# Performance work log

Measured on AMD Instinct MI355X. Metric: run time of the kernel, lower is better.

The kernel has to match this reference:

```python
import jax, jax.numpy as jnp
import numpy as np

N_NODES = 50000
F_IN = 96
HIDDEN = 128
OUT = 64
N_EDGES = 800000


def setup_inputs() -> dict:
    key = jax.random.key(0)
    ks = jax.random.split(key, 8)
    x = jax.random.normal(ks[0], (N_NODES, F_IN), dtype=jnp.float32)
    edge_index = jax.random.randint(ks[1], (2, N_EDGES), 0, N_NODES, dtype=jnp.int64)
    s = 1.0 / np.sqrt(F_IN)
    W1_rel = jax.random.uniform(ks[2], (HIDDEN, F_IN), minval=-s, maxval=s, dtype=jnp.float32)
    b1 = jax.random.uniform(ks[3], (HIDDEN,), minval=-s, maxval=s, dtype=jnp.float32)
    W1_root = jax.random.uniform(ks[4], (HIDDEN, F_IN), minval=-s, maxval=s, dtype=jnp.float32)
    s2 = 1.0 / np.sqrt(HIDDEN)
    W2_rel = jax.random.uniform(ks[5], (OUT, HIDDEN), minval=-s2, maxval=s2, dtype=jnp.float32)
    b2 = jax.random.uniform(ks[6], (OUT,), minval=-s2, maxval=s2, dtype=jnp.float32)
    W2_root = jax.random.uniform(ks[7], (OUT, HIDDEN), minval=-s2, maxval=s2, dtype=jnp.float32)
    return {"x": x, "edge_index": edge_index, "W1_rel": W1_rel, "b1": b1,
            "W1_root": W1_root, "W2_rel": W2_rel, "b2": b2, "W2_root": W2_root}


def _graph_conv(x, src, dst, mask, W_rel, b, W_root):
    # messages = x[src] (masked to remove self-loops), sum-aggregated at dst
    msgs = x[src] * mask  # [E, F]
    agg = jax.ops.segment_sum(msgs, dst, num_segments=x.shape[0])  # [N, F]
    return agg @ W_rel.T + b + x @ W_root.T


def reference(x, edge_index, W1_rel, b1, W1_root, W2_rel, b2, W2_root):
    src, dst = edge_index[0], edge_index[1]
    # remove_self_loops: zero out contributions of edges with src == dst
    mask = (src != dst).astype(x.dtype)[:, None]  # [E, 1]
    h = jax.nn.relu(_graph_conv(x, src, dst, mask, W1_rel, b1, W1_root))
    out = _graph_conv(h, src, dst, mask, W2_rel, b2, W2_root)
    return out
```

## Files before the change

### kernel.cpp

```cpp
#include <hip/hip_runtime.h>


#define N_NODES 50000
#define F_IN    96
#define HIDDEN  128
#define OUT_F   64
#define DCAP    64

typedef __attribute__((ext_vector_type(8))) short short8;
typedef __attribute__((ext_vector_type(4))) float floatx4;

__device__ inline unsigned short f2bf(float f) {
    union { float f; unsigned u; } v; v.f = f;
    unsigned r = v.u + 0x7FFF + ((v.u >> 16) & 1);
    return (unsigned short)(r >> 16);
}
__device__ inline float bf2f(unsigned short b) {
    union { unsigned u; float f; } v; v.u = ((unsigned)b) << 16;
    return v.f;
}

__global__ __launch_bounds__(256) void setup_place_kernel(
    const float* __restrict__ x,
    const float* __restrict__ W1_rel, const float* __restrict__ W1_root,
    const float* __restrict__ W2_rel, const float* __restrict__ W2_root,
    const int* __restrict__ ei,
    unsigned short* __restrict__ xb, unsigned short* __restrict__ W1b,
    unsigned short* __restrict__ W2rb, unsigned short* __restrict__ W2sb,
    int* __restrict__ deg, int* __restrict__ csr,
    int SB, int total8, int E, int slice_size)
{
    const int tid = threadIdx.x;
    if ((int)blockIdx.x < SB) {
        int i = blockIdx.x * 256 + tid;
        if (i < total8) {
            const float4* p = (const float4*)(x + (size_t)i * 8);
            float4 v0 = p[0], v1 = p[1];
            short8 o;
            o[0] = (short)f2bf(v0.x); o[1] = (short)f2bf(v0.y);
            o[2] = (short)f2bf(v0.z); o[3] = (short)f2bf(v0.w);
            o[4] = (short)f2bf(v1.x); o[5] = (short)f2bf(v1.y);
            o[6] = (short)f2bf(v1.z); o[7] = (short)f2bf(v1.w);
            *(short8*)(xb + (size_t)i * 8) = o;
        }
        if (i < 128 * 192) {
            int j = i / 192, k = i % 192;
            float v = (k < 96) ? W1_rel[j * 96 + k] : W1_root[j * 96 + k - 96];
            W1b[i] = f2bf(v);
        } else if (i < 128 * 192 + 64 * 128) {
            int i2 = i - 128 * 192;
            W2rb[i2] = f2bf(W2_rel[i2]);
        } else if (i < 128 * 192 + 2 * 64 * 128) {
            int i3 = i - 128 * 192 - 64 * 128;
            W2sb[i3] = f2bf(W2_root[i3]);
        }
        return;
    }
    int pb = blockIdx.x - SB;
    int sl = pb & 7;
    int i4 = (pb >> 3) * 256 + tid;
    int E4 = E >> 2;
    if (i4 < E4) {
        int4 d4 = ((const int4*)(ei + E))[i4];
        int e0 = i4 * 4;
        int dd[4] = {d4.x, d4.y, d4.z, d4.w};
        #pragma unroll
        for (int k = 0; k < 4; ++k) {
            int d = dd[k];
            if ((unsigned)d >= (unsigned)N_NODES) continue;
            if (d / slice_size != sl) continue;
            int s = ei[e0 + k];
            if (s == d) continue;
            int r = atomicAdd(&deg[d], 1);
            if (r < DCAP) csr[d * DCAP + r] = s;
        }
    } else if (i4 == E4) {
        for (int e = E4 * 4; e < E; ++e) {
            int d = ei[E + e];
            if ((unsigned)d >= (unsigned)N_NODES) continue;
            if (d / slice_size != sl) continue;
            int s = ei[e];
            if (s == d) continue;
            int r = atomicAdd(&deg[d], 1);
            if (r < DCAP) csr[d * DCAP + r] = s;
        }
    }
}

template<int F>
__device__ inline void gather_row8(const unsigned short* __restrict__ feat,
                                   const int* __restrict__ csr, int j, int end,
                                   float* acc)
{
    const unsigned short* fc = feat;
    for (; j + 3 < end; j += 4) {
        int s0 = csr[j], s1 = csr[j + 1], s2 = csr[j + 2], s3 = csr[j + 3];
        s0 = ((unsigned)s0 < (unsigned)N_NODES) ? s0 : 0;
        s1 = ((unsigned)s1 < (unsigned)N_NODES) ? s1 : 0;
        s2 = ((unsigned)s2 < (unsigned)N_NODES) ? s2 : 0;
        s3 = ((unsigned)s3 < (unsigned)N_NODES) ? s3 : 0;
        short8 v0 = *(const short8*)(fc + (size_t)s0 * F);
        short8 v1 = *(const short8*)(fc + (size_t)s1 * F);
        short8 v2 = *(const short8*)(fc + (size_t)s2 * F);
        short8 v3 = *(const short8*)(fc + (size_t)s3 * F);
        #pragma unroll
        for (int i = 0; i < 8; ++i)
            acc[i] += (bf2f((unsigned short)v0[i]) + bf2f((unsigned short)v1[i]))
                    + (bf2f((unsigned short)v2[i]) + bf2f((unsigned short)v3[i]));
    }
    for (; j < end; ++j) {
        int s0 = csr[j];
        s0 = ((unsigned)s0 < (unsigned)N_NODES) ? s0 : 0;
        short8 v0 = *(const short8*)(fc + (size_t)s0 * F);
        #pragma unroll
        for (int i = 0; i < 8; ++i) acc[i] += bf2f((unsigned short)v0[i]);
    }
}

__global__ __launch_bounds__(256) void mega1_kernel(
    const unsigned short* __restrict__ xb, const unsigned short* __restrict__ W1b,
    const unsigned short* __restrict__ W2rb, const float* __restrict__ b1,
    const int* __restrict__ deg, const int* __restrict__ csr,
    unsigned short* __restrict__ h, unsigned short* __restrict__ t, int N)
{
    __shared__ __align__(16) unsigned short aggs[32][104];
    __shared__ __align__(16) unsigned short hs[32][136];
    const int tid = threadIdx.x;
    const int node0 = blockIdx.x * 32;

    for (int task = tid; task < 384; task += 256) {
        int nl = task / 12, c = task % 12;
        int node = node0 + nl;
        float acc[8] = {};
        if (node < N) {
            int dg = deg[node];
            if (dg > DCAP) dg = DCAP;
            int j = node * DCAP;
            gather_row8<F_IN>(xb + c * 8, csr, j, j + dg, acc);
        }
        short8 o;
        #pragma unroll
        for (int i = 0; i < 8; ++i) o[i] = (short)f2bf(acc[i]);
        *(short8*)&aggs[nl][c * 8] = o;
    }
    __syncthreads();

    const int lane = tid & 63;
    const int wave = tid >> 6;
    const int m = lane & 15, quad = lane >> 4;
    const int nh = wave & 1;
    const int node_base = node0 + nh * 16;
    const int jt0 = (wave >> 1) * 4;
    int na = node_base + m;
    if (na >= N) na = N - 1;
    short8 a[6];
    #pragma unroll
    for (int c = 0; c < 3; ++c)
        a[c] = *(const short8*)&aggs[nh * 16 + m][c * 32 + quad * 8];
    #pragma unroll
    for (int c = 0; c < 3; ++c)
        a[3 + c] = *(const short8*)(xb + (size_t)na * 96 + c * 32 + quad * 8);
    #pragma unroll
    for (int jt = 0; jt < 4; ++jt) {
        floatx4 acc = {0.f, 0.f, 0.f, 0.f};
        const unsigned short* wb = W1b + (size_t)((jt0 + jt) * 16 + m) * 192 + quad * 8;
        #pragma unroll
        for (int c = 0; c < 6; ++c) {
            short8 b = *(const short8*)(wb + c * 32);
            acc = __builtin_amdgcn_mfma_f32_16x16x32_bf16(a[c], b, acc, 0, 0, 0);
        }
        int col = (jt0 + jt) * 16 + m;
        float bv = b1[col];
        #pragma unroll
        for (int r = 0; r < 4; ++r) {
            int node = node_base + quad * 4 + r;
            float v = fmaxf(acc[r] + bv, 0.f);
            unsigned short vb = f2bf(v);
            hs[nh * 16 + quad * 4 + r][col] = vb;
            if (node < N) h[(size_t)node * 128 + col] = vb;
        }
    }
    __syncthreads();

    const int jtt0 = (wave >> 1) * 2;
    short8 a2[4];
    #pragma unroll
    for (int c = 0; c < 4; ++c)
        a2[c] = *(const short8*)&hs[nh * 16 + m][c * 32 + quad * 8];
    #pragma unroll
    for (int jt = 0; jt < 2; ++jt) {
        floatx4 acc = {0.f, 0.f, 0.f, 0.f};
        const unsigned short* wb = W2rb + (size_t)((jtt0 + jt) * 16 + m) * 128 + quad * 8;
        #pragma unroll
        for (int c = 0; c < 4; ++c) {
            short8 b = *(const short8*)(wb + c * 32);
            acc = __builtin_amdgcn_mfma_f32_16x16x32_bf16(a2[c], b, acc, 0, 0, 0);
        }
        int col = (jtt0 + jt) * 16 + m;
        #pragma unroll
        for (int r = 0; r < 4; ++r) {
            int node = node_base + quad * 4 + r;
            if (node < N)
                t[(size_t)node * 64 + col] = f2bf(acc[r]);
        }
    }
}

__global__ __launch_bounds__(256) void gemm3_fused(
    const unsigned short* __restrict__ h, const unsigned short* __restrict__ tfeat,
    const unsigned short* __restrict__ W2sb, const float* __restrict__ b2,
    const int* __restrict__ deg, const int* __restrict__ csr,
    float* __restrict__ out, int N)
{
    __shared__ __align__(16) unsigned short agg2s[32][72];
    const int tid = threadIdx.x;
    const int node0 = blockIdx.x * 32;

    {
        int nl = tid / 8, c = tid % 8;
        int node = node0 + nl;
        float acc[8] = {};
        if (node < N) {
            int dg = deg[node];
            if (dg > DCAP) dg = DCAP;
            int j = node * DCAP;
            gather_row8<OUT_F>(tfeat + c * 8, csr, j, j + dg, acc);
        }
        short8 o;
        #pragma unroll
        for (int i = 0; i < 8; ++i) o[i] = (short)f2bf(acc[i]);
        *(short8*)&agg2s[nl][c * 8] = o;
    }
    __syncthreads();

    const int lane = tid & 63;
    const int wave = tid >> 6;
    const int m = lane & 15, quad = lane >> 4;
    const int node_base = node0 + (wave & 1) * 16;
    const int jt0 = (wave >> 1) * 2;
    int na = node_base + m;
    if (na >= N) na = N - 1;
    short8 a[4];
    #pragma unroll
    for (int c = 0; c < 4; ++c)
        a[c] = *(const short8*)(h + (size_t)na * 128 + c * 32 + quad * 8);
    #pragma unroll
    for (int jt = 0; jt < 2; ++jt) {
        floatx4 acc = {0.f, 0.f, 0.f, 0.f};
        const unsigned short* wb = W2sb + (size_t)((jt0 + jt) * 16 + m) * 128 + quad * 8;
        #pragma unroll
        for (int c = 0; c < 4; ++c) {
            short8 b = *(const short8*)(wb + c * 32);
            acc = __builtin_amdgcn_mfma_f32_16x16x32_bf16(a[c], b, acc, 0, 0, 0);
        }
        int col = (jt0 + jt) * 16 + m;
        float bv = b2[col];
        #pragma unroll
        for (int r = 0; r < 4; ++r) {
            int node = node_base + quad * 4 + r;
            if (node < N) {
                int nl = (wave & 1) * 16 + quad * 4 + r;
                float v = acc[r] + bv + bf2f(agg2s[nl][col]);
                out[(size_t)node * 64 + col] = v;
            }
        }
    }
}

extern "C" void kernel_launch(void* const* d_in, const int* in_sizes, int n_in,
                              void* d_out, int out_size, void* d_ws, size_t ws_size,
                              hipStream_t stream) {
    const float* x       = (const float*)d_in[0];
    const int*   ei      = (const int*)d_in[1];
    const float* W1_rel  = (const float*)d_in[2];
    const float* b1      = (const float*)d_in[3];
    const float* W1_root = (const float*)d_in[4];
    const float* W2_rel  = (const float*)d_in[5];
    const float* b2      = (const float*)d_in[6];
    const float* W2_root = (const float*)d_in[7];
    float* out = (float*)d_out;

    const int N = in_sizes[0] / F_IN;
    const int E = in_sizes[1] / 2;
    const int slice_size = ((N + 2047) / 2048) * 256;

    char* ws = (char*)d_ws;
    size_t p = 0;
    unsigned short* xb   = (unsigned short*)(ws + p); p += (size_t)N_NODES * F_IN * 2;
    unsigned short* h    = (unsigned short*)(ws + p); p += (size_t)N_NODES * HIDDEN * 2;
    unsigned short* t    = (unsigned short*)(ws + p); p += (size_t)N_NODES * OUT_F * 2;
    unsigned short* W1b  = (unsigned short*)(ws + p); p += (size_t)128 * 192 * 2;
    unsigned short* W2rb = (unsigned short*)(ws + p); p += (size_t)64 * 128 * 2;
    unsigned short* W2sb = (unsigned short*)(ws + p); p += (size_t)64 * 128 * 2;
    int* deg = (int*)(ws + p);  p += (size_t)N_NODES * 4;
    int* csr = (int*)(ws + p);  p += (size_t)N_NODES * DCAP * 4;

    hipMemsetAsync(deg, 0, (size_t)N * 4, stream);

    {
        int total8 = N * F_IN / 8;
        int SB = (total8 + 255) / 256;
        int E4 = E >> 2;
        int bps = (E4 + 1 + 255) / 256;
        int PB = bps * 8;
        setup_place_kernel<<<SB + PB, 256, 0, stream>>>(
            x, W1_rel, W1_root, W2_rel, W2_root, ei,
            xb, W1b, W2rb, W2sb, deg, csr, SB, total8, E, slice_size);
    }

    const int tiles32 = (N + 31) / 32;

    mega1_kernel<<<tiles32, 256, 0, stream>>>(xb, W1b, W2rb, b1, deg, csr, h, t, N);

    gemm3_fused<<<tiles32, 256, 0, stream>>>(h, t, W2sb, b2, deg, csr, out, N);
}
```

Baseline: 201.0 us.

## Split gathers into XCD-aware kernels over 32-column feature slabs

Feature matrices are stored a second time as 32-column slabs, and the neighbor gathers move into a separate kernel. That kernel maps each XCD (via blockIdx & 7) to one slab, so each XCD's L2 holds a smaller working set of 3.2 MB rather than the full table. Each node's neighbor list is now split across 4 lanes and combined with shuffles, and csr indices are read with nontemporal loads. The cost is two extra kernel launches, extra global round trips for the aggregate buffers and a duplicated copy of x.

```diff
diff --git a/kernel.cpp b/kernel.cpp
--- a/kernel.cpp
+++ b/kernel.cpp
@@ -25,7 +25,8 @@
     const float* __restrict__ W1_rel, const float* __restrict__ W1_root,
     const float* __restrict__ W2_rel, const float* __restrict__ W2_root,
     const int* __restrict__ ei,
-    unsigned short* __restrict__ xb, unsigned short* __restrict__ W1b,
+    unsigned short* __restrict__ xb, unsigned short* __restrict__ xc,
+    unsigned short* __restrict__ W1b,
     unsigned short* __restrict__ W2rb, unsigned short* __restrict__ W2sb,
     int* __restrict__ deg, int* __restrict__ csr,
     int SB, int total8, int E, int slice_size)
@@ -42,6 +43,9 @@
             o[4] = (short)f2bf(v1.x); o[5] = (short)f2bf(v1.y);
             o[6] = (short)f2bf(v1.z); o[7] = (short)f2bf(v1.w);
             *(short8*)(xb + (size_t)i * 8) = o;
+            int node = i / 12, c = i % 12;
+            int slab = c >> 2, c2 = c & 3;
+            *(short8*)(xc + ((size_t)slab * N_NODES + node) * 32 + c2 * 8) = o;
         }
         if (i < 128 * 192) {
             int j = i / 192, k = i % 192;
@@ -87,64 +91,75 @@
     }
 }
 
-template<int F>
-__device__ inline void gather_row8(const unsigned short* __restrict__ feat,
-                                   const int* __restrict__ csr, int j, int end,
-                                   float* acc)
+template<int OUTSTRIDE>
+__global__ __launch_bounds__(512) void gather_kernel(
+    const unsigned short* __restrict__ fc,
+    const int* __restrict__ deg, const int* __restrict__ csr,
+    unsigned short* __restrict__ aggout, int N, int three_slabs)
 {
-    const unsigned short* fc = feat;
-    for (; j + 3 < end; j += 4) {
-        int s0 = csr[j], s1 = csr[j + 1], s2 = csr[j + 2], s3 = csr[j + 3];
-        s0 = ((unsigned)s0 < (unsigned)N_NODES) ? s0 : 0;
-        s1 = ((unsigned)s1 < (unsigned)N_NODES) ? s1 : 0;
-        s2 = ((unsigned)s2 < (unsigned)N_NODES) ? s2 : 0;
-        s3 = ((unsigned)s3 < (unsigned)N_NODES) ? s3 : 0;
-        short8 v0 = *(const short8*)(fc + (size_t)s0 * F);
-        short8 v1 = *(const short8*)(fc + (size_t)s1 * F);
-        short8 v2 = *(const short8*)(fc + (size_t)s2 * F);
-        short8 v3 = *(const short8*)(fc + (size_t)s3 * F);
-        #pragma unroll
-        for (int i = 0; i < 8; ++i)
-            acc[i] += (bf2f((unsigned short)v0[i]) + bf2f((unsigned short)v1[i]))
-                    + (bf2f((unsigned short)v2[i]) + bf2f((unsigned short)v3[i]));
-    }
-    for (; j < end; ++j) {
-        int s0 = csr[j];
-        s0 = ((unsigned)s0 < (unsigned)N_NODES) ? s0 : 0;
-        short8 v0 = *(const short8*)(fc + (size_t)s0 * F);
-        #pragma unroll
-        for (int i = 0; i < 8; ++i) acc[i] += bf2f((unsigned short)v0[i]);
-    }
-}
-
-__global__ __launch_bounds__(256) void mega1_kernel(
-    const unsigned short* __restrict__ xb, const unsigned short* __restrict__ W1b,
-    const unsigned short* __restrict__ W2rb, const float* __restrict__ b1,
-    const int* __restrict__ deg, const int* __restrict__ csr,
-    unsigned short* __restrict__ h, unsigned short* __restrict__ t, int N)
+    const int tid = threadIdx.x;
+    const int bid = blockIdx.x;
+    const int xcd = bid & 7;
+    const int k = bid >> 3;
+    int slab, rank, g;
+    if (three_slabs) { slab = xcd % 3; rank = xcd / 3; g = (slab == 2) ? 2 : 3; }
+    else             { slab = xcd & 1; rank = xcd >> 1; g = 4; }
+    const int ntiles = (N + 31) >> 5;
+    const int tile = k * g + rank;
+    if (tile >= ntiles) return;
+
+    const int c2 = tid & 3;
+    const int q  = (tid >> 2) & 3;
+    const int nl = tid >> 4;
+    const int node = tile * 32 + nl;
+    const unsigned short* sb = fc + (size_t)slab * N_NODES * 32 + c2 * 8;
+
+    float acc[8] = {};
+    if (node < N) {
+        int dg = deg[node]; if (dg > DCAP) dg = DCAP;
+        int j = node * DCAP + q;
+        const int end = node * DCAP + dg;
+        for (; j + 4 < end; j += 8) {
+            int s0 = __builtin_nontemporal_load(csr + j);
+            int s1 = __builtin_nontemporal_load(csr + j + 4);
+            s0 = ((unsigned)s0 < (unsigned)N_NODES) ? s0 : 0;
+            s1 = ((unsigned)s1 < (unsigned)N_NODES) ? s1 : 0;
+            short8 v0 = *(const short8*)(sb + (size_t)s0 * 32);
+            short8 v1 = *(const short8*)(sb + (size_t)s1 * 32);
+            #pragma unroll
+            for (int i = 0; i < 8; ++i)
+                acc[i] += bf2f((unsigned short)v0[i]) + bf2f((unsigned short)v1[i]);
+        }
+        if (j < end) {
+            int s0 = __builtin_nontemporal_load(csr + j);
+            s0 = ((unsigned)s0 < (unsigned)N_NODES) ? s0 : 0;
+            short8 v0 = *(const short8*)(sb + (size_t)s0 * 32);
+            #pragma unroll
+            for (int i = 0; i < 8; ++i) acc[i] += bf2f((unsigned short)v0[i]);
+        }
+    }
+    #pragma unroll
+    for (int i = 0; i < 8; ++i) {
+        acc[i] += __shfl_xor(acc[i], 4);
+        acc[i] += __shfl_xor(acc[i], 8);
+    }
+    if (q == 0 && node < N) {
+        short8 o;
+        #pragma unroll
+        for (int i = 0; i < 8; ++i) o[i] = (short)f2bf(acc[i]);
+        *(short8*)(aggout + (size_t)node * OUTSTRIDE + slab * 32 + c2 * 8) = o;
+    }
+}
+
+__global__ __launch_bounds__(256) void gemm12_kernel(
+    const unsigned short* __restrict__ xb, const unsigned short* __restrict__ aggb,
+    const unsigned short* __restrict__ W1b, const unsigned short* __restrict__ W2rb,
+    const float* __restrict__ b1,
+    unsigned short* __restrict__ h, unsigned short* __restrict__ tc, int N)
 {
-    __shared__ __align__(16) unsigned short aggs[32][104];
     __shared__ __align__(16) unsigned short hs[32][136];
     const int tid = threadIdx.x;
     const int node0 = blockIdx.x * 32;
-
-    for (int task = tid; task < 384; task += 256) {
-        int nl = task / 12, c = task % 12;
-        int node = node0 + nl;
-        float acc[8] = {};
-        if (node < N) {
-            int dg = deg[node];
-            if (dg > DCAP) dg = DCAP;
-            int j = node * DCAP;
-            gather_row8<F_IN>(xb + c * 8, csr, j, j + dg, acc);
-        }
-        short8 o;
-        #pragma unroll
-        for (int i = 0; i < 8; ++i) o[i] = (short)f2bf(acc[i]);
-        *(short8*)&aggs[nl][c * 8] = o;
-    }
-    __syncthreads();
-
     const int lane = tid & 63;
     const int wave = tid >> 6;
     const int m = lane & 15, quad = lane >> 4;
@@ -156,7 +171,7 @@
     short8 a[6];
     #pragma unroll
     for (int c = 0; c < 3; ++c)
-        a[c] = *(const short8*)&aggs[nh * 16 + m][c * 32 + quad * 8];
+        a[c] = *(const short8*)(aggb + (size_t)na * 96 + c * 32 + quad * 8);
     #pragma unroll
     for (int c = 0; c < 3; ++c)
         a[3 + c] = *(const short8*)(xb + (size_t)na * 96 + c * 32 + quad * 8);
@@ -197,42 +212,23 @@
             acc = __builtin_amdgcn_mfma_f32_16x16x32_bf16(a2[c], b, acc, 0, 0, 0);
         }
         int col = (jtt0 + jt) * 16 + m;
+        int slab = col >> 5, cw = col & 31;
         #pragma unroll
         for (int r = 0; r < 4; ++r) {
             int node = node_base + quad * 4 + r;
             if (node < N)
-                t[(size_t)node * 64 + col] = f2bf(acc[r]);
-        }
-    }
-}
-
-__global__ __launch_bounds__(256) void gemm3_fused(
-    const unsigned short* __restrict__ h, const unsigned short* __restrict__ tfeat,
+                tc[((size_t)slab * N_NODES + node) * 32 + cw] = f2bf(acc[r]);
+        }
+    }
+}
+
+__global__ __launch_bounds__(256) void gemm3_kernel(
+    const unsigned short* __restrict__ h, const unsigned short* __restrict__ agg2b,
     const unsigned short* __restrict__ W2sb, const float* __restrict__ b2,
-    const int* __restrict__ deg, const int* __restrict__ csr,
     float* __restrict__ out, int N)
 {
-    __shared__ __align__(16) unsigned short agg2s[32][72];
     const int tid = threadIdx.x;
     const int node0 = blockIdx.x * 32;
-
-    {
-        int nl = tid / 8, c = tid % 8;
-        int node = node0 + nl;
-        float acc[8] = {};
-        if (node < N) {
-            int dg = deg[node];
-            if (dg > DCAP) dg = DCAP;
-            int j = node * DCAP;
-            gather_row8<OUT_F>(tfeat + c * 8, csr, j, j + dg, acc);
-        }
-        short8 o;
-        #pragma unroll
-        for (int i = 0; i < 8; ++i) o[i] = (short)f2bf(acc[i]);
-        *(short8*)&agg2s[nl][c * 8] = o;
-    }
-    __syncthreads();
-
     const int lane = tid & 63;
     const int wave = tid >> 6;
     const int m = lane & 15, quad = lane >> 4;
@@ -244,6 +240,17 @@
     #pragma unroll
     for (int c = 0; c < 4; ++c)
         a[c] = *(const short8*)(h + (size_t)na * 128 + c * 32 + quad * 8);
+    float agv[2][4];
+    #pragma unroll
+    for (int jt = 0; jt < 2; ++jt) {
+        int col = (jt0 + jt) * 16 + m;
+        #pragma unroll
+        for (int r = 0; r < 4; ++r) {
+            int node = node_base + quad * 4 + r;
+            int nc = (node < N) ? node : (N - 1);
+            agv[jt][r] = bf2f(agg2b[(size_t)nc * 64 + col]);
+        }
+    }
     #pragma unroll
     for (int jt = 0; jt < 2; ++jt) {
         floatx4 acc = {0.f, 0.f, 0.f, 0.f};
@@ -258,11 +265,8 @@
         #pragma unroll
         for (int r = 0; r < 4; ++r) {
             int node = node_base + quad * 4 + r;
-            if (node < N) {
-                int nl = (wave & 1) * 16 + quad * 4 + r;
-                float v = acc[r] + bv + bf2f(agg2s[nl][col]);
-                out[(size_t)node * 64 + col] = v;
-            }
+            if (node < N)
+                out[(size_t)node * 64 + col] = acc[r] + bv + agv[jt][r];
         }
     }
 }
@@ -286,12 +290,15 @@
 
     char* ws = (char*)d_ws;
     size_t p = 0;
-    unsigned short* xb   = (unsigned short*)(ws + p); p += (size_t)N_NODES * F_IN * 2;
-    unsigned short* h    = (unsigned short*)(ws + p); p += (size_t)N_NODES * HIDDEN * 2;
-    unsigned short* t    = (unsigned short*)(ws + p); p += (size_t)N_NODES * OUT_F * 2;
-    unsigned short* W1b  = (unsigned short*)(ws + p); p += (size_t)128 * 192 * 2;
-    unsigned short* W2rb = (unsigned short*)(ws + p); p += (size_t)64 * 128 * 2;
-    unsigned short* W2sb = (unsigned short*)(ws + p); p += (size_t)64 * 128 * 2;
+    unsigned short* xb    = (unsigned short*)(ws + p); p += (size_t)N_NODES * F_IN * 2;
+    unsigned short* xc    = (unsigned short*)(ws + p); p += (size_t)3 * N_NODES * 32 * 2;
+    unsigned short* aggb  = (unsigned short*)(ws + p); p += (size_t)N_NODES * F_IN * 2;
+    unsigned short* h     = (unsigned short*)(ws + p); p += (size_t)N_NODES * HIDDEN * 2;
+    unsigned short* tc    = (unsigned short*)(ws + p); p += (size_t)2 * N_NODES * 32 * 2;
+    unsigned short* agg2b = (unsigned short*)(ws + p); p += (size_t)N_NODES * OUT_F * 2;
+    unsigned short* W1b   = (unsigned short*)(ws + p); p += (size_t)128 * 192 * 2;
+    unsigned short* W2rb  = (unsigned short*)(ws + p); p += (size_t)64 * 128 * 2;
+    unsigned short* W2sb  = (unsigned short*)(ws + p); p += (size_t)64 * 128 * 2;
     int* deg = (int*)(ws + p);  p += (size_t)N_NODES * 4;
     int* csr = (int*)(ws + p);  p += (size_t)N_NODES * DCAP * 4;
 
@@ -305,12 +312,22 @@
         int PB = bps * 8;
         setup_place_kernel<<<SB + PB, 256, 0, stream>>>(
             x, W1_rel, W1_root, W2_rel, W2_root, ei,
-            xb, W1b, W2rb, W2sb, deg, csr, SB, total8, E, slice_size);
-    }
-
-    const int tiles32 = (N + 31) / 32;
-
-    mega1_kernel<<<tiles32, 256, 0, stream>>>(xb, W1b, W2rb, b1, deg, csr, h, t, N);
-
-    gemm3_fused<<<tiles32, 256, 0, stream>>>(h, t, W2sb, b2, deg, csr, out, N);
-}
+            xb, xc, W1b, W2rb, W2sb, deg, csr, SB, total8, E, slice_size);
+    }
+
+    const int ntiles = (N + 31) / 32;
+
+    {
+        int g1k = (ntiles + 1) / 2;
+        gather_kernel<96><<<8 * g1k, 512, 0, stream>>>(xc, deg, csr, aggb, N, 1);
+    }
+
+    gemm12_kernel<<<ntiles, 256, 0, stream>>>(xb, aggb, W1b, W2rb, b1, h, tc, N);
+
+    {
+        int g2k = (ntiles + 3) / 4;
+        gather_kernel<64><<<8 * g2k, 512, 0, stream>>>(tc, deg, csr, agg2b, N, 0);
+    }
+
+    gemm3_kernel<<<ntiles, 256, 0, stream>>>(h, agg2b, W2sb, b2, out, N);
+}
```

Measured after the change: 234.3 us. 1.17x slower.

## Pack edge pairs into 16-bit words and store CSR indices as uint16

Applied to the files above, without the earlier changes.

Adds a pre-pass kernel that packs each (src,dst) pair into one 32-bit word and zeroes the degree array, which replaces the memset. The 8 placement slices then each read one packed array instead of the 64-bit index arrays, and the CSR neighbour lists are stored as 16-bit indices. Both gather kernels read half as many index bytes. This relies on N fitting in 16 bits (50000 < 65536), writes an extra packed buffer, and adds one kernel launch.

```diff
diff --git a/kernel.cpp b/kernel.cpp
--- a/kernel.cpp
+++ b/kernel.cpp
@@ -20,14 +20,47 @@
     return v.f;
 }
 
+__global__ __launch_bounds__(256) void pack_zero_kernel(
+    const int* __restrict__ ei, unsigned* __restrict__ pd,
+    int* __restrict__ deg, int E, int N)
+{
+    const int i = blockIdx.x * 256 + threadIdx.x;
+    const int E4 = E >> 2;
+    if (i < E4) {
+        int4 s4 = ((const int4*)ei)[i];
+        int4 d4 = ((const int4*)(ei + E))[i];
+        int ss[4] = {s4.x, s4.y, s4.z, s4.w};
+        int dd[4] = {d4.x, d4.y, d4.z, d4.w};
+        unsigned o[4];
+        #pragma unroll
+        for (int k = 0; k < 4; ++k) {
+            unsigned s = (unsigned)ss[k], d = (unsigned)dd[k];
+            if (s >= (unsigned)N || d >= (unsigned)N) { s = 0; d = 0; }
+            o[k] = s | (d << 16);
+        }
+        uint4 ov; ov.x = o[0]; ov.y = o[1]; ov.z = o[2]; ov.w = o[3];
+        ((uint4*)pd)[i] = ov;
+    } else if (i == E4) {
+        for (int e = E4 * 4; e < E; ++e) {
+            unsigned s = (unsigned)ei[e], d = (unsigned)ei[E + e];
+            if (s >= (unsigned)N || d >= (unsigned)N) { s = 0; d = 0; }
+            pd[e] = s | (d << 16);
+        }
+    }
+    if (i < (N >> 2)) {
+        int4 z; z.x = 0; z.y = 0; z.z = 0; z.w = 0;
+        ((int4*)deg)[i] = z;
+    }
+}
+
 __global__ __launch_bounds__(256) void setup_place_kernel(
     const float* __restrict__ x,
     const float* __restrict__ W1_rel, const float* __restrict__ W1_root,
     const float* __restrict__ W2_rel, const float* __restrict__ W2_root,
-    const int* __restrict__ ei,
+    const unsigned* __restrict__ pd,
     unsigned short* __restrict__ xb, unsigned short* __restrict__ W1b,
     unsigned short* __restrict__ W2rb, unsigned short* __restrict__ W2sb,
-    int* __restrict__ deg, int* __restrict__ csr,
+    int* __restrict__ deg, unsigned short* __restrict__ csr,
     int SB, int total8, int E, int slice_size)
 {
     const int tid = threadIdx.x;
@@ -58,47 +91,41 @@
     }
     int pb = blockIdx.x - SB;
     int sl = pb & 7;
+    unsigned lo = (unsigned)(sl * slice_size);
     int i4 = (pb >> 3) * 256 + tid;
     int E4 = E >> 2;
     if (i4 < E4) {
-        int4 d4 = ((const int4*)(ei + E))[i4];
-        int e0 = i4 * 4;
-        int dd[4] = {d4.x, d4.y, d4.z, d4.w};
+        uint4 p4 = ((const uint4*)pd)[i4];
+        unsigned pp[4] = {p4.x, p4.y, p4.z, p4.w};
         #pragma unroll
         for (int k = 0; k < 4; ++k) {
-            int d = dd[k];
-            if ((unsigned)d >= (unsigned)N_NODES) continue;
-            if (d / slice_size != sl) continue;
-            int s = ei[e0 + k];
+            unsigned s = pp[k] & 0xFFFFu, d = pp[k] >> 16;
+            if (d - lo >= (unsigned)slice_size) continue;
             if (s == d) continue;
             int r = atomicAdd(&deg[d], 1);
-            if (r < DCAP) csr[d * DCAP + r] = s;
+            if (r < DCAP) csr[(size_t)d * DCAP + r] = (unsigned short)s;
         }
     } else if (i4 == E4) {
         for (int e = E4 * 4; e < E; ++e) {
-            int d = ei[E + e];
-            if ((unsigned)d >= (unsigned)N_NODES) continue;
-            if (d / slice_size != sl) continue;
-            int s = ei[e];
+            unsigned s = pd[e] & 0xFFFFu, d = pd[e] >> 16;
+            if (d - lo >= (unsigned)slice_size) continue;
             if (s == d) continue;
             int r = atomicAdd(&deg[d], 1);
-            if (r < DCAP) csr[d * DCAP + r] = s;
+            if (r < DCAP) csr[(size_t)d * DCAP + r] = (unsigned short)s;
         }
     }
 }
 
 template<int F>
 __device__ inline void gather_row8(const unsigned short* __restrict__ feat,
-                                   const int* __restrict__ csr, int j, int end,
-                                   float* acc)
+                                   const unsigned short* __restrict__ csr,
+                                   int j, int end, float* acc)
 {
     const unsigned short* fc = feat;
     for (; j + 3 < end; j += 4) {
-        int s0 = csr[j], s1 = csr[j + 1], s2 = csr[j + 2], s3 = csr[j + 3];
-        s0 = ((unsigned)s0 < (unsigned)N_NODES) ? s0 : 0;
-        s1 = ((unsigned)s1 < (unsigned)N_NODES) ? s1 : 0;
-        s2 = ((unsigned)s2 < (unsigned)N_NODES) ? s2 : 0;
-        s3 = ((unsigned)s3 < (unsigned)N_NODES) ? s3 : 0;
+        uint2 cs = *(const uint2*)(csr + j);
+        int s0 = cs.x & 0xFFFF, s1 = cs.x >> 16;
+        int s2 = cs.y & 0xFFFF, s3 = cs.y >> 16;
         short8 v0 = *(const short8*)(fc + (size_t)s0 * F);
         short8 v1 = *(const short8*)(fc + (size_t)s1 * F);
         short8 v2 = *(const short8*)(fc + (size_t)s2 * F);
@@ -110,7 +137,6 @@
     }
     for (; j < end; ++j) {
         int s0 = csr[j];
-        s0 = ((unsigned)s0 < (unsigned)N_NODES) ? s0 : 0;
         short8 v0 = *(const short8*)(fc + (size_t)s0 * F);
         #pragma unroll
         for (int i = 0; i < 8; ++i) acc[i] += bf2f((unsigned short)v0[i]);
@@ -120,7 +146,7 @@
 __global__ __launch_bounds__(256) void mega1_kernel(
     const unsigned short* __restrict__ xb, const unsigned short* __restrict__ W1b,
     const unsigned short* __restrict__ W2rb, const float* __restrict__ b1,
-    const int* __restrict__ deg, const int* __restrict__ csr,
+    const int* __restrict__ deg, const unsigned short* __restrict__ csr,
     unsigned short* __restrict__ h, unsigned short* __restrict__ t, int N)
 {
     __shared__ __align__(16) unsigned short aggs[32][104];
@@ -209,7 +235,7 @@
 __global__ __launch_bounds__(256) void gemm3_fused(
     const unsigned short* __restrict__ h, const unsigned short* __restrict__ tfeat,
     const unsigned short* __restrict__ W2sb, const float* __restrict__ b2,
-    const int* __restrict__ deg, const int* __restrict__ csr,
+    const int* __restrict__ deg, const unsigned short* __restrict__ csr,
     float* __restrict__ out, int N)
 {
     __shared__ __align__(16) unsigned short agg2s[32][72];
@@ -292,19 +318,25 @@
     unsigned short* W1b  = (unsigned short*)(ws + p); p += (size_t)128 * 192 * 2;
     unsigned short* W2rb = (unsigned short*)(ws + p); p += (size_t)64 * 128 * 2;
     unsigned short* W2sb = (unsigned short*)(ws + p); p += (size_t)64 * 128 * 2;
-    int* deg = (int*)(ws + p);  p += (size_t)N_NODES * 4;
-    int* csr = (int*)(ws + p);  p += (size_t)N_NODES * DCAP * 4;
-
-    hipMemsetAsync(deg, 0, (size_t)N * 4, stream);
+    int* deg = (int*)(ws + p);            p += ((size_t)N_NODES + 16) * 4;
+    unsigned short* csr = (unsigned short*)(ws + p); p += (size_t)N_NODES * DCAP * 2;
+    unsigned* pd = (unsigned*)(ws + p);   p += (size_t)800000 * 4;
+
+    const int E4 = E >> 2;
+
+    {
+        int work = (E4 + 1 > (N >> 2)) ? (E4 + 1) : (N >> 2);
+        int PZ = (work + 255) / 256;
+        pack_zero_kernel<<<PZ, 256, 0, stream>>>(ei, pd, deg, E, N);
+    }
 
     {
         int total8 = N * F_IN / 8;
         int SB = (total8 + 255) / 256;
-        int E4 = E >> 2;
         int bps = (E4 + 1 + 255) / 256;
         int PB = bps * 8;
         setup_place_kernel<<<SB + PB, 256, 0, stream>>>(
-            x, W1_rel, W1_root, W2_rel, W2_root, ei,
+            x, W1_rel, W1_root, W2_rel, W2_root, pd,
             xb, W1b, W2rb, W2sb, deg, csr, SB, total8, E, slice_size);
     }
 
```

After: 197.8 us. Within noise of the previous version (-1.6%).
